# Optimization experiments

Hardware: AMD Instinct MI355X
Metric: run time of the kernel (lower is better)

The kernel has to match this reference:

```python
import jax, jax.numpy as jnp
import numpy as np

HIDDEN = 2048
NUM_HEADS = 16
NUM_KV_HEADS = 8
HEAD_DIM = 128
Q_SIZE = NUM_HEADS * HEAD_DIM          # 2048
KV_SIZE = NUM_KV_HEADS * HEAD_DIM      # 1024
ROPE_THETA = 1000000.0
RMS_EPS = 1e-6
SCALE = HEAD_DIM ** -0.5


def setup_inputs() -> dict:
    key = jax.random.key(0)
    k1, k2, k3 = jax.random.split(key, 3)
    T = 4096
    positions = jnp.arange(T, dtype=jnp.int64) if jax.config.jax_enable_x64 else jnp.arange(T, dtype=jnp.int32)
    hidden_states = jax.random.normal(k1, (T, HIDDEN), dtype=jnp.float32)
    qkv_w = jax.random.normal(k2, (Q_SIZE + 2 * KV_SIZE, HIDDEN), dtype=jnp.float32) * 0.02
    o_w = jax.random.normal(k3, (HIDDEN, Q_SIZE), dtype=jnp.float32) * 0.02
    q_norm_w = jnp.ones((HEAD_DIM,), dtype=jnp.float32)
    k_norm_w = jnp.ones((HEAD_DIM,), dtype=jnp.float32)
    return {
        "hidden_states": hidden_states,
        "qkv_w": qkv_w,
        "q_norm_w": q_norm_w,
        "k_norm_w": k_norm_w,
        "o_w": o_w,
        "positions": positions,
    }


def _rms_norm(x, w, eps=RMS_EPS):
    # per-head RMSNorm over last dim (head_dim)
    var = jnp.mean(jnp.square(x), axis=-1, keepdims=True)
    return x * jax.lax.rsqrt(var + eps) * w


def _rope(x, positions):
    # neox-style (rotate-half) RoPE. x: [T, H, D], positions: [T]
    D = x.shape[-1]
    inv_freq = 1.0 / (ROPE_THETA ** (jnp.arange(0, D, 2, dtype=jnp.float32) / D))  # [D/2]
    freqs = positions.astype(jnp.float32)[:, None] * inv_freq                      # [T, D/2]
    cos = jnp.cos(freqs)[:, None, :]  # [T, 1, D/2]
    sin = jnp.sin(freqs)[:, None, :]
    x1, x2 = x[..., : D // 2], x[..., D // 2 :]
    return jnp.concatenate([x1 * cos - x2 * sin, x2 * cos + x1 * sin], axis=-1)


def reference(hidden_states, qkv_w, q_norm_w, k_norm_w, o_w, positions):
    T = hidden_states.shape[0]
    qkv = hidden_states @ qkv_w.T                                   # [T, Q+2KV]
    q = qkv[:, :Q_SIZE].reshape(T, NUM_HEADS, HEAD_DIM)
    k = qkv[:, Q_SIZE : Q_SIZE + KV_SIZE].reshape(T, NUM_KV_HEADS, HEAD_DIM)
    v = qkv[:, Q_SIZE + KV_SIZE :].reshape(T, NUM_KV_HEADS, HEAD_DIM)

    # attention_bias=False path: per-head QK RMSNorm
    q = _rms_norm(q, q_norm_w)
    k = _rms_norm(k, k_norm_w)

    q = _rope(q, positions)
    k = _rope(k, positions)

    # GQA: expand KV heads to query heads
    rep = NUM_HEADS // NUM_KV_HEADS
    k = jnp.repeat(k, rep, axis=1)   # [T, H, D]
    v = jnp.repeat(v, rep, axis=1)

    scores = jnp.einsum("qhd,khd->hqk", q, k) * SCALE               # [H, T, T]
    causal = positions[:, None] >= positions[None, :]               # [T, T]
    scores = jnp.where(causal[None], scores, jnp.finfo(scores.dtype).min)
    probs = jax.nn.softmax(scores, axis=-1)
    attn = jnp.einsum("hqk,khd->qhd", probs, v)                     # [T, H, D]
    return attn.reshape(T, Q_SIZE) @ o_w.T                          # [T, HIDDEN]
```

## Files before the change

kernel.cpp:

```cpp
#include <hip/hip_runtime.h>
#include <hip/hip_bf16.h>
#include <math.h>


typedef __bf16 bf16;
typedef __bf16 bf16x4 __attribute__((ext_vector_type(4)));
typedef __bf16 bf16x8 __attribute__((ext_vector_type(8)));
typedef float  f32x4  __attribute__((ext_vector_type(4)));

__device__ __forceinline__ f32x4 mfma16(bf16x8 a, bf16x8 b, f32x4 c) {
  return __builtin_amdgcn_mfma_f32_16x16x32_bf16(a, b, c, 0, 0, 0);
}

__device__ __forceinline__ void mfma16x16_chain4(const bf16x4& a0, const bf16x4& a1,
                                                 const bf16x4& a2, const bf16x4& a3,
                                                 const bf16x4& b0, const bf16x4& b1,
                                                 const bf16x4& b2, const bf16x4& b3,
                                                 f32x4& c) {
  asm volatile(
      "s_nop 2\n\t"
      "v_mfma_f32_16x16x16_bf16 %0, %1, %5, %0\n\t"
      "v_mfma_f32_16x16x16_bf16 %0, %2, %6, %0\n\t"
      "v_mfma_f32_16x16x16_bf16 %0, %3, %7, %0\n\t"
      "v_mfma_f32_16x16x16_bf16 %0, %4, %8, %0"
      : "+v"(c)
      : "v"(a0), "v"(a1), "v"(a2), "v"(a3),
        "v"(b0), "v"(b1), "v"(b2), "v"(b3));
}

__device__ __forceinline__ void gload_lds16(const bf16* g, bf16* l) {
  __builtin_amdgcn_global_load_lds(
      (const __attribute__((address_space(1))) unsigned int*)g,
      (__attribute__((address_space(3))) unsigned int*)l, 16, 0, 0);
}

__device__ __forceinline__ void store_c(float* p, float v) { *p = v; }
__device__ __forceinline__ void store_c(bf16* p, float v) { *p = (bf16)v; }

__global__ __launch_bounds__(256) void cast_bf16(const float* __restrict__ s,
                                                 bf16* __restrict__ d) {
  int i = blockIdx.x * 256 + threadIdx.x;
  float4 a = reinterpret_cast<const float4*>(s)[i * 2];
  float4 b = reinterpret_cast<const float4*>(s)[i * 2 + 1];
  bf16x8 v = {(bf16)a.x, (bf16)a.y, (bf16)a.z, (bf16)a.w,
              (bf16)b.x, (bf16)b.y, (bf16)b.z, (bf16)b.w};
  reinterpret_cast<bf16x8*>(d)[i] = v;
}

__device__ __forceinline__ void gemm_step(const bf16* AsL, const bf16* BsL,
                                          int wm, int wn, int l16, int quad,
                                          f32x4 (&acc)[4][4]) {
  bf16x8 af[4], bfr[4];
#pragma unroll
  for (int i = 0; i < 4; ++i)
    af[i] = *reinterpret_cast<const bf16x8*>(&AsL[(wm + i * 16 + l16) * 32 + quad * 8]);
#pragma unroll
  for (int j = 0; j < 4; ++j)
    bfr[j] = *reinterpret_cast<const bf16x8*>(&BsL[(wn + j * 16 + l16) * 32 + quad * 8]);
#pragma unroll
  for (int i = 0; i < 4; ++i)
#pragma unroll
    for (int j = 0; j < 4; ++j)
      acc[i][j] = mfma16(af[i], bfr[j], acc[i][j]);
}

template <typename TC>
__global__ __launch_bounds__(256, 4) void gemm_bt(const bf16* __restrict__ A,
                                                  const bf16* __restrict__ B,
                                                  TC* __restrict__ C,
                                                  int M, int N, int K) {
  __shared__ __align__(16) bf16 As[2][128 * 32];
  __shared__ __align__(16) bf16 Bs[2][128 * 32];

  const int tid  = threadIdx.x;
  const int wave = tid >> 6, lane = tid & 63;
  const int quad = lane >> 4, l16 = lane & 15;
  const int wm = (wave >> 1) * 64, wn = (wave & 1) * 64;
  const int n0 = blockIdx.x * 128, m0 = blockIdx.y * 128;

  const int r0 = tid >> 2;
  const int c0 = (tid & 3) * 8;
  const size_t aBase = (size_t)(m0 + r0) * K + c0;
  const size_t bBase = (size_t)(n0 + r0) * K + c0;
  const size_t rowK64 = (size_t)64 * K;

  const f32x4 zero = {0.f, 0.f, 0.f, 0.f};
  f32x4 acc[4][4];
#pragma unroll
  for (int i = 0; i < 4; ++i)
#pragma unroll
    for (int j = 0; j < 4; ++j) acc[i][j] = zero;

  gload_lds16(&A[aBase],          &As[0][tid * 8]);
  gload_lds16(&A[aBase + rowK64], &As[0][2048 + tid * 8]);
  gload_lds16(&B[bBase],          &Bs[0][tid * 8]);
  gload_lds16(&B[bBase + rowK64], &Bs[0][2048 + tid * 8]);
  __syncthreads();

  int cur = 0;
  for (int k0 = 32; k0 < K; k0 += 32) {
    const int nb = cur ^ 1;
    gload_lds16(&A[aBase + k0],          &As[nb][tid * 8]);
    gload_lds16(&A[aBase + rowK64 + k0], &As[nb][2048 + tid * 8]);
    gload_lds16(&B[bBase + k0],          &Bs[nb][tid * 8]);
    gload_lds16(&B[bBase + rowK64 + k0], &Bs[nb][2048 + tid * 8]);

    gemm_step(As[cur], Bs[cur], wm, wn, l16, quad, acc);

    __syncthreads();
    cur = nb;
  }
  gemm_step(As[cur], Bs[cur], wm, wn, l16, quad, acc);

#pragma unroll
  for (int i = 0; i < 4; ++i)
#pragma unroll
    for (int j = 0; j < 4; ++j)
#pragma unroll
      for (int r = 0; r < 4; ++r) {
        int row = m0 + wm + i * 16 + quad * 4 + r;
        int col = n0 + wn + j * 16 + l16;
        store_c(&C[(size_t)row * N + col], acc[i][j][r]);
      }
}

__global__ __launch_bounds__(128) void norm_rope(const bf16* __restrict__ qkv,
                                                 const float* __restrict__ qw,
                                                 const float* __restrict__ kw,
                                                 const int* __restrict__ pos,
                                                 bf16* __restrict__ qn,
                                                 bf16* __restrict__ kn) {
  const int t   = blockIdx.x;
  const int hr  = blockIdx.y;
  const int tid = threadIdx.x;
  const bool isq = hr < 16;
  const int col  = isq ? hr * 128 : 2048 + (hr - 16) * 128;

  float x = (float)qkv[(size_t)t * 4096 + col + tid];
  float ss = x * x;
#pragma unroll
  for (int o = 32; o >= 1; o >>= 1) ss += __shfl_xor(ss, o);
  __shared__ float part[2];
  __shared__ float sh[128];
  if ((tid & 63) == 0) part[tid >> 6] = ss;
  __syncthreads();
  float total = part[0] + part[1];
  float rms = rsqrtf(total * (1.0f / 128.0f) + 1e-6f);
  const float* w = isq ? qw : kw;
  float xn = x * rms * w[tid];
  sh[tid] = xn;
  __syncthreads();

  int d = tid & 63;
  float inv = exp2f((float)d * (-19.93156856932417f / 64.0f));
  float fr = (float)pos[t] * inv;
  float sn, cs;
  sincosf(fr, &sn, &cs);
  float out = (tid < 64) ? (sh[tid] * cs - sh[tid + 64] * sn)
                         : (sh[tid] * cs + sh[tid - 64] * sn);
  if (isq) qn[(size_t)t * 2048 + hr * 128 + tid] = (bf16)out;
  else     kn[(size_t)t * 1024 + (hr - 16) * 128 + tid] = (bf16)out;
}

__global__ __launch_bounds__(256) void transpose_v(const bf16* __restrict__ qkv,
                                                   bf16* __restrict__ vt) {
  __shared__ __align__(16) bf16 tile[128 * 72];
  const int t0 = blockIdx.x * 64, kvh = blockIdx.y;
  const int tid = threadIdx.x;
#pragma unroll
  for (int it = 0; it < 2; ++it) {
    int linear = it * 4096 + tid * 16;
    int r = linear >> 7, c = linear & 127;
    union { uint4 v; bf16 e[8]; } u0, u1;
    u0.v = *reinterpret_cast<const uint4*>(
        &qkv[(size_t)(t0 + r) * 4096 + 3072 + kvh * 128 + c]);
    u1.v = *reinterpret_cast<const uint4*>(
        &qkv[(size_t)(t0 + r) * 4096 + 3072 + kvh * 128 + c + 8]);
#pragma unroll
    for (int j = 0; j < 8; ++j) tile[(c + j) * 72 + r] = u0.e[j];
#pragma unroll
    for (int j = 0; j < 8; ++j) tile[(c + 8 + j) * 72 + r] = u1.e[j];
  }
  __syncthreads();
#pragma unroll
  for (int it = 0; it < 4; ++it) {
    int linear = it * 2048 + tid * 8;
    int d = linear >> 6, c = linear & 63;
    uint4 v = *reinterpret_cast<const uint4*>(&tile[d * 72 + c]);
    *reinterpret_cast<uint4*>(&vt[(size_t)(kvh * 128 + d) * 4096 + t0 + c]) = v;
  }
}

__global__ __launch_bounds__(256, 2) void attn(const bf16* __restrict__ q,
                                               const bf16* __restrict__ k,
                                               const bf16* __restrict__ vt,
                                               bf16* __restrict__ out) {
  __shared__ __align__(16) bf16 Ks[2][64 * 128];
  __shared__ __align__(16) bf16 Vs[2][128 * 64];

  const int head = blockIdx.y, kvh = head >> 1;
  const int bx = blockIdx.x;

  const int tid = threadIdx.x;
  const int wave = tid >> 6, lane = tid & 63;
  const int quad = lane >> 4, l16 = lane & 15;
  const float cExp = 0.08838834764831845f * 1.4426950408889634f;
  const f32x4 zero = {0.f, 0.f, 0.f, 0.f};

  int kSrc[4], vSrc[4];
#pragma unroll
  for (int it = 0; it < 4; ++it) {
    int r = (wave * 4 + it) * 4 + (lane >> 4);
    kSrc[it] = r * 1024 + kvh * 128 + (((lane & 15) ^ (r & 7)) << 3);
    int d = (wave * 4 + it) * 8 + (lane >> 3);
    vSrc[it] = (kvh * 128 + d) * 4096 + (((lane & 7) ^ (lane >> 3)) << 3);
  }

  const int kswz = (l16 & 7) << 3;
  int koff[4], voff[4];
#pragma unroll
  for (int s = 0; s < 4; ++s) {
    koff[s] = (s * 32 + quad * 8) ^ kswz;
    voff[s] = (s * 16 + quad * 4) ^ kswz;
  }

#pragma unroll
  for (int it = 0; it < 4; ++it) {
    gload_lds16(&k[kSrc[it]], &Ks[0][(wave * 4 + it) * 512]);
    gload_lds16(&vt[vSrc[it]], &Vs[0][(wave * 4 + it) * 512]);
  }
  int cur = 0;

#pragma unroll
  for (int phase = 0; phase < 2; ++phase) {
    const int qt = phase == 0 ? bx : 63 - bx;
    const int q0 = qt * 64;
    const int kend = q0 + 64;
    const int qrow = q0 + wave * 16 + l16;

    bf16x8 qf[4];
#pragma unroll
    for (int s = 0; s < 4; ++s)
      qf[s] = *reinterpret_cast<const bf16x8*>(
          &q[(size_t)qrow * 2048 + head * 128 + s * 32 + quad * 8]);

    f32x4 o_acc[8];
#pragma unroll
    for (int dt = 0; dt < 8; ++dt) o_acc[dt] = zero;
    float m_i = -3.0e38f, l_i = 0.f;

    for (int k0 = 0; k0 < kend; k0 += 64) {
      __syncthreads();

      int nk0 = -1;
      if (k0 + 64 < kend)     nk0 = k0 + 64;
      else if (phase == 0)    nk0 = 0;
      if (nk0 >= 0) {
#pragma unroll
        for (int it = 0; it < 4; ++it) {
          gload_lds16(&k[kSrc[it] + nk0 * 1024],
                      &Ks[cur ^ 1][(wave * 4 + it) * 512]);
          gload_lds16(&vt[vSrc[it] + nk0],
                      &Vs[cur ^ 1][(wave * 4 + it) * 512]);
        }
      }

      const bf16* KsL = Ks[cur];
      const bf16* VsL = Vs[cur];

      f32x4 s_acc[4];
      __builtin_amdgcn_s_setprio(1);
#pragma unroll
      for (int mt = 0; mt < 4; ++mt) {
        bf16x8 kf[4];
#pragma unroll
        for (int ks = 0; ks < 4; ++ks)
          kf[ks] = *reinterpret_cast<const bf16x8*>(
              &KsL[(mt * 16 + l16) * 128 + koff[ks]]);
        f32x4 sa = zero;
#pragma unroll
        for (int ks = 0; ks < 4; ++ks) sa = mfma16(kf[ks], qf[ks], sa);
        s_acc[mt] = sa;
      }
      __builtin_amdgcn_s_setprio(0);

      if (k0 == q0) {
        int tq = wave * 16 + l16;
#pragma unroll
        for (int mt = 0; mt < 4; ++mt)
#pragma unroll
          for (int r = 0; r < 4; ++r) {
            int tk = mt * 16 + quad * 4 + r;
            if (tk > tq) s_acc[mt][r] = -3.0e38f;
          }
      }

      {
        float mx = -3.0e38f;
#pragma unroll
        for (int mt = 0; mt < 4; ++mt)
#pragma unroll
          for (int r = 0; r < 4; ++r) mx = fmaxf(mx, s_acc[mt][r]);
        mx = fmaxf(mx, __shfl_xor(mx, 16));
        mx = fmaxf(mx, __shfl_xor(mx, 32));
        if (!__all((mx - m_i) * cExp <= 8.0f)) {
          float mn = fmaxf(m_i, mx);
          float al = exp2f((m_i - mn) * cExp);
          m_i = mn;
          l_i *= al;
#pragma unroll
          for (int dt = 0; dt < 8; ++dt)
#pragma unroll
            for (int r = 0; r < 4; ++r) o_acc[dt][r] *= al;
        }
        float nmc = -m_i * cExp;
        float rs = 0.f;
#pragma unroll
        for (int mt = 0; mt < 4; ++mt)
#pragma unroll
          for (int r = 0; r < 4; ++r) {
            float pe = exp2f(fmaf(s_acc[mt][r], cExp, nmc));
            s_acc[mt][r] = pe;
            rs += pe;
          }
        rs += __shfl_xor(rs, 16);
        rs += __shfl_xor(rs, 32);
        l_i += rs;
      }

      bf16x4 pb[4];
#pragma unroll
      for (int mt = 0; mt < 4; ++mt) {
        bf16x4 t;
#pragma unroll
        for (int r = 0; r < 4; ++r) t[r] = (bf16)s_acc[mt][r];
        pb[mt] = t;
      }

      __builtin_amdgcn_s_setprio(1);
#pragma unroll
      for (int dt = 0; dt < 8; ++dt) {
        const bf16* vrow = &VsL[(dt * 16 + l16) * 64];
        bf16x4 va0 = *reinterpret_cast<const bf16x4*>(&vrow[voff[0]]);
        bf16x4 va1 = *reinterpret_cast<const bf16x4*>(&vrow[voff[1]]);
        bf16x4 va2 = *reinterpret_cast<const bf16x4*>(&vrow[voff[2]]);
        bf16x4 va3 = *reinterpret_cast<const bf16x4*>(&vrow[voff[3]]);
        mfma16x16_chain4(va0, va1, va2, va3, pb[0], pb[1], pb[2], pb[3],
                         o_acc[dt]);
      }
      __builtin_amdgcn_s_setprio(0);
      cur ^= 1;
    }

    float rl = __builtin_amdgcn_rcpf(l_i);
#pragma unroll
    for (int dt = 0; dt < 8; ++dt) {
      bf16x4 ov;
#pragma unroll
      for (int r = 0; r < 4; ++r) ov[r] = (bf16)(o_acc[dt][r] * rl);
      *reinterpret_cast<bf16x4*>(
          &out[(size_t)qrow * 2048 + head * 128 + dt * 16 + quad * 4]) = ov;
    }
  }
}

extern "C" void kernel_launch(void* const* d_in, const int* in_sizes, int n_in,
                              void* d_out, int out_size, void* d_ws, size_t ws_size,
                              hipStream_t stream) {
  const float* hidden = (const float*)d_in[0];
  const float* qkv_w  = (const float*)d_in[1];
  const float* qnw    = (const float*)d_in[2];
  const float* knw    = (const float*)d_in[3];
  const float* o_w    = (const float*)d_in[4];
  const int*   pos    = (const int*)d_in[5];

  bf16* qkv = (bf16*)d_ws;
  bf16* qn  = qkv + (size_t)4096 * 4096;
  bf16* kn  = qn  + (size_t)4096 * 2048;
  bf16* vt  = kn  + (size_t)4096 * 1024;
  bf16* ao  = vt  + (size_t)1024 * 4096;
  bf16* hb  = ao;
  bf16* wq  = kn;
  bf16* wo  = qn;
  float* out = (float*)d_out;

  cast_bf16<<<4096, 256, 0, stream>>>(hidden, hb);
  cast_bf16<<<4096, 256, 0, stream>>>(qkv_w, wq);
  gemm_bt<<<dim3(32, 32), 256, 0, stream>>>(hb, wq, qkv, 4096, 4096, 2048);
  norm_rope<<<dim3(4096, 24), 128, 0, stream>>>(qkv, qnw, knw, pos, qn, kn);
  transpose_v<<<dim3(64, 8), 256, 0, stream>>>(qkv, vt);
  attn<<<dim3(32, 16), 256, 0, stream>>>(qn, kn, vt, ao);
  cast_bf16<<<2048, 256, 0, stream>>>(o_w, wo);
  gemm_bt<<<dim3(16, 32), 256, 0, stream>>>(ao, wo, out, 4096, 2048, 2048);
}
```

Before: 426.4 us.

## Use 256x256 triple-buffered GEMM for QKV projection and per-token norm_rope

Adds a new GEMM kernel with 256x256 output tiles, 512 threads, a three-stage LDS ring buffer fed by direct global-to-LDS loads, and an XCD-aware block swizzle, and uses it for the QKV projection. The larger tiles raise data reuse per LDS load and the deeper prefetch hides memory latency. The norm_rope kernel is also restructured so each block handles one token across all 24 heads, with one wave per six heads and warp-shuffle reductions. This removes shared-memory barriers and recomputes sin/cos once per token instead of once per head. The big tile uses a lot of registers and LDS, which limits occupancy, and gives only 256 workgroups.

```diff
diff --git a/kernel.cpp b/kernel.cpp
--- a/kernel.cpp
+++ b/kernel.cpp
@@ -47,6 +47,103 @@
   reinterpret_cast<bf16x8*>(d)[i] = v;
 }
 
+__global__ __launch_bounds__(512, 2) void gemm256(const bf16* __restrict__ A,
+                                                  const bf16* __restrict__ B,
+                                                  bf16* __restrict__ C,
+                                                  int M, int N, int K) {
+  __shared__ __align__(16) bf16 As[3][256 * 32];
+  __shared__ __align__(16) bf16 Bs[3][256 * 32];
+
+  const int tid  = threadIdx.x;
+  const int lane = tid & 63;
+  const int wid  = tid >> 6;
+  const int quad = lane >> 4, l16 = lane & 15;
+  const int wr = wid >> 2, wc = wid & 3;
+
+  const int nbx = N >> 8;
+  const int nwg = (M >> 8) * nbx;
+  const int cpx = nwg >> 3;
+  const int swz = (blockIdx.x & 7) * cpx + (blockIdx.x >> 3);
+  const int m0 = (swz / nbx) << 8;
+  const int n0 = (swz % nbx) << 8;
+
+  const int srow = tid >> 2, scol = (tid & 3) * 8;
+  const bf16* aSrc0 = &A[(size_t)(m0 + srow) * K + scol];
+  const bf16* aSrc1 = &A[(size_t)(m0 + 128 + srow) * K + scol];
+  const bf16* bSrc0 = &B[(size_t)(n0 + srow) * K + scol];
+  const bf16* bSrc1 = &B[(size_t)(n0 + 128 + srow) * K + scol];
+
+  const f32x4 zero = {0.f, 0.f, 0.f, 0.f};
+  f32x4 acc[8][4];
+#pragma unroll
+  for (int i = 0; i < 8; ++i)
+#pragma unroll
+    for (int j = 0; j < 4; ++j) acc[i][j] = zero;
+
+  const int NT = K >> 5;
+
+  {
+    gload_lds16(aSrc0, &As[0][tid * 8]);
+    gload_lds16(aSrc1, &As[0][4096 + tid * 8]);
+    gload_lds16(bSrc0, &Bs[0][tid * 8]);
+    gload_lds16(bSrc1, &Bs[0][4096 + tid * 8]);
+    gload_lds16(aSrc0 + 32, &As[1][tid * 8]);
+    gload_lds16(aSrc1 + 32, &As[1][4096 + tid * 8]);
+    gload_lds16(bSrc0 + 32, &Bs[1][tid * 8]);
+    gload_lds16(bSrc1 + 32, &Bs[1][4096 + tid * 8]);
+  }
+
+  int bufC = 0;
+  for (int t = 0; t < NT; ++t) {
+    if (t == NT - 1) {
+      asm volatile("s_waitcnt vmcnt(0)" ::: "memory");
+    } else {
+      asm volatile("s_waitcnt vmcnt(4)" ::: "memory");
+    }
+    __builtin_amdgcn_s_barrier();
+    __builtin_amdgcn_sched_barrier(0);
+
+    if (t + 2 < NT) {
+      int bs = bufC + 2; if (bs >= 3) bs -= 3;
+      const int k0 = (t + 2) * 32;
+      gload_lds16(aSrc0 + k0, &As[bs][tid * 8]);
+      gload_lds16(aSrc1 + k0, &As[bs][4096 + tid * 8]);
+      gload_lds16(bSrc0 + k0, &Bs[bs][tid * 8]);
+      gload_lds16(bSrc1 + k0, &Bs[bs][4096 + tid * 8]);
+    }
+
+    const bf16* AsL = As[bufC];
+    const bf16* BsL = Bs[bufC];
+    bf16x8 af[8], bfv[4];
+#pragma unroll
+    for (int fm = 0; fm < 8; ++fm)
+      af[fm] = *reinterpret_cast<const bf16x8*>(
+          &AsL[(wr * 128 + fm * 16 + l16) * 32 + quad * 8]);
+#pragma unroll
+    for (int fn = 0; fn < 4; ++fn)
+      bfv[fn] = *reinterpret_cast<const bf16x8*>(
+          &BsL[(wc * 64 + fn * 16 + l16) * 32 + quad * 8]);
+#pragma unroll
+    for (int fm = 0; fm < 8; ++fm)
+#pragma unroll
+      for (int fn = 0; fn < 4; ++fn)
+        acc[fm][fn] = mfma16(af[fm], bfv[fn], acc[fm][fn]);
+
+    bufC = bufC + 1 == 3 ? 0 : bufC + 1;
+  }
+
+#pragma unroll
+  for (int fm = 0; fm < 8; ++fm)
+#pragma unroll
+    for (int fn = 0; fn < 4; ++fn)
+#pragma unroll
+      for (int r = 0; r < 4; ++r) {
+        int row = m0 + wr * 128 + fm * 16 + quad * 4 + r;
+        int col = n0 + wc * 64 + fn * 16 + l16;
+        C[(size_t)row * N + col] = (bf16)acc[fm][fn][r];
+      }
+}
+
 __device__ __forceinline__ void gemm_step(const bf16* AsL, const bf16* BsL,
                                           int wm, int wn, int l16, int quad,
                                           f32x4 (&acc)[4][4]) {
@@ -124,42 +221,46 @@
       }
 }
 
-__global__ __launch_bounds__(128) void norm_rope(const bf16* __restrict__ qkv,
+__global__ __launch_bounds__(256) void norm_rope(const bf16* __restrict__ qkv,
                                                  const float* __restrict__ qw,
                                                  const float* __restrict__ kw,
                                                  const int* __restrict__ pos,
                                                  bf16* __restrict__ qn,
                                                  bf16* __restrict__ kn) {
-  const int t   = blockIdx.x;
-  const int hr  = blockIdx.y;
-  const int tid = threadIdx.x;
-  const bool isq = hr < 16;
-  const int col  = isq ? hr * 128 : 2048 + (hr - 16) * 128;
-
-  float x = (float)qkv[(size_t)t * 4096 + col + tid];
-  float ss = x * x;
-#pragma unroll
-  for (int o = 32; o >= 1; o >>= 1) ss += __shfl_xor(ss, o);
-  __shared__ float part[2];
-  __shared__ float sh[128];
-  if ((tid & 63) == 0) part[tid >> 6] = ss;
-  __syncthreads();
-  float total = part[0] + part[1];
-  float rms = rsqrtf(total * (1.0f / 128.0f) + 1e-6f);
-  const float* w = isq ? qw : kw;
-  float xn = x * rms * w[tid];
-  sh[tid] = xn;
-  __syncthreads();
-
-  int d = tid & 63;
-  float inv = exp2f((float)d * (-19.93156856932417f / 64.0f));
+  const int t = blockIdx.x;
+  const int wv = threadIdx.x >> 6, l = threadIdx.x & 63;
+
+  float inv = exp2f((float)l * (-19.93156856932417f / 64.0f));
   float fr = (float)pos[t] * inv;
   float sn, cs;
   sincosf(fr, &sn, &cs);
-  float out = (tid < 64) ? (sh[tid] * cs - sh[tid + 64] * sn)
-                         : (sh[tid] * cs + sh[tid - 64] * sn);
-  if (isq) qn[(size_t)t * 2048 + hr * 128 + tid] = (bf16)out;
-  else     kn[(size_t)t * 1024 + (hr - 16) * 128 + tid] = (bf16)out;
+  const float qw1 = qw[l], qw2 = qw[l + 64];
+  const float kw1 = kw[l], kw2 = kw[l + 64];
+  const size_t rowb = (size_t)t * 4096;
+
+#pragma unroll
+  for (int i = 0; i < 6; ++i) {
+    const int h = wv * 6 + i;
+    const bool isq = h < 16;
+    const int col = isq ? h * 128 : 2048 + (h - 16) * 128;
+    float x1 = (float)qkv[rowb + col + l];
+    float x2 = (float)qkv[rowb + col + l + 64];
+    float ss = x1 * x1 + x2 * x2;
+#pragma unroll
+    for (int o = 32; o >= 1; o >>= 1) ss += __shfl_xor(ss, o);
+    float rms = rsqrtf(ss * (1.0f / 128.0f) + 1e-6f);
+    float w1 = isq ? qw1 : kw1, w2 = isq ? qw2 : kw2;
+    float xn1 = x1 * rms * w1, xn2 = x2 * rms * w2;
+    float o1 = xn1 * cs - xn2 * sn;
+    float o2 = xn2 * cs + xn1 * sn;
+    if (isq) {
+      qn[(size_t)t * 2048 + h * 128 + l] = (bf16)o1;
+      qn[(size_t)t * 2048 + h * 128 + l + 64] = (bf16)o2;
+    } else {
+      kn[(size_t)t * 1024 + (h - 16) * 128 + l] = (bf16)o1;
+      kn[(size_t)t * 1024 + (h - 16) * 128 + l + 64] = (bf16)o2;
+    }
+  }
 }
 
 __global__ __launch_bounds__(256) void transpose_v(const bf16* __restrict__ qkv,
@@ -386,8 +487,8 @@
 
   cast_bf16<<<4096, 256, 0, stream>>>(hidden, hb);
   cast_bf16<<<4096, 256, 0, stream>>>(qkv_w, wq);
-  gemm_bt<<<dim3(32, 32), 256, 0, stream>>>(hb, wq, qkv, 4096, 4096, 2048);
-  norm_rope<<<dim3(4096, 24), 128, 0, stream>>>(qkv, qnw, knw, pos, qn, kn);
+  gemm256<<<256, 512, 0, stream>>>(hb, wq, qkv, 4096, 4096, 2048);
+  norm_rope<<<4096, 256, 0, stream>>>(qkv, qnw, knw, pos, qn, kn);
   transpose_v<<<dim3(64, 8), 256, 0, stream>>>(qkv, vt);
   attn<<<dim3(32, 16), 256, 0, stream>>>(qn, kn, vt, ao);
   cast_bf16<<<2048, 256, 0, stream>>>(o_w, wo);
```

Result: faster. 417.4 us (-2.1%).
